# Optimization experiments

Measured on AMD Instinct MI355X. Metric: run time of the kernel, lower is better.

The kernel has to match this reference:

```python
import jax, jax.numpy as jnp
import numpy as np


def setup_inputs() -> dict:
    key = jax.random.key(0)
    B, S, D = 8, 2048, 1024
    inputs = jax.random.normal(key, (B, S, D), dtype=jnp.float32)
    return {"inputs": inputs}


def reference(inputs):
    # scores = X X^T / seq_len  (source divides by dk = inputs.shape[-2], the seq dim)
    seq_len = inputs.shape[-2]
    scores = jnp.einsum('bsd,btd->bst', inputs, inputs) / seq_len
    scores = jax.nn.softmax(scores, axis=-1)
    # context is computed in the original but not returned; keep the matmul for fidelity
    context = jnp.einsum('bst,btd->bsd', scores, inputs)
    del context
    return (inputs, scores)
```

## Files before the change

### kernel.cpp

```cpp
#include <hip/hip_runtime.h>

typedef unsigned short ushort_t;
using short8 = __attribute__((ext_vector_type(8))) short;
using half4  = __attribute__((ext_vector_type(4))) _Float16;
using half8  = __attribute__((ext_vector_type(8))) _Float16;
using f32x4  = __attribute__((ext_vector_type(4))) float;

#define AS1 __attribute__((address_space(1)))
#define AS3 __attribute__((address_space(3)))

#define B_   8
#define S_   2048
#define D_   1024
#define NIN  (8UL * 2048UL * 1024UL)
#define PARTS 32
#define SROWB 8192UL
#define BATCHB (2048UL * SROWB)


__device__ __forceinline__ ushort_t f2bf(float f) {
    unsigned u = __float_as_uint(f);
    u += 0x7FFFu + ((u >> 16) & 1u);
    return (ushort_t)(u >> 16);
}

__global__ __launch_bounds__(256) void cvt_packed(const float* __restrict__ in,
                                                  char* sc) {
    size_t g = ((size_t)blockIdx.x * 256 + threadIdx.x) * 8;
    const float4* p = (const float4*)(in + g);
    float4 a = p[0], c = p[1];
    short8 r;
    r[0] = (short)f2bf(a.x); r[1] = (short)f2bf(a.y);
    r[2] = (short)f2bf(a.z); r[3] = (short)f2bf(a.w);
    r[4] = (short)f2bf(c.x); r[5] = (short)f2bf(c.y);
    r[6] = (short)f2bf(c.z); r[7] = (short)f2bf(c.w);
    size_t xrow = g >> 10;
    size_t col  = g & 1023;
    char* dst = sc + xrow * SROWB + 2048 + col * 2;
    *(short8*)dst = r;
}

__global__ __launch_bounds__(256, 2) void gemm_sym3(char* sc,
                                                    const float4* xin,
                                                    float4* xout) {
    __shared__ __align__(16) ushort_t sA[2][128 * 64];
    __shared__ __align__(16) ushort_t sB[2][128 * 64];

    const int lin = blockIdx.x;
    const int wg  = (lin & 7) * 136 + (lin >> 3);
    const int b   = wg / 136;
    int rem = wg % 136, ti = 0;
    while (rem >= 16 - ti) { rem -= 16 - ti; ++ti; }
    const int tj = ti + rem;
    const int tr = ti * 128, tc = tj * 128;

    char* Sb = sc + (size_t)b * BATCHB;

    const int tid  = threadIdx.x;
    const int lane = tid & 63;
    const int wid  = tid >> 6;
    const int wr = (wid >> 1) * 64;
    const int wc = (wid & 1) * 64;

    const bool docopy = (lin < 1024);
    const size_t cbase = (size_t)lin * 256 + tid;

    f32x4 acc[4][4] = {};
    float4 creg;

    const int srow_s = tid >> 3;
    const int cd     = tid & 7;
    const int rsel = lane & 15;
    const int g4   = lane >> 4;
    const int sw   = lane & 7;

    auto stage = [&](int s, int slot) {
#pragma unroll
        for (int j = 0; j < 4; ++j) {
            const int row = j * 32 + srow_s;
            const int csw = (cd ^ (row & 7)) << 4;
            const size_t rbA = (size_t)(tr + row) * SROWB + 2048 + (size_t)s * 128;
            const size_t rbB = (size_t)(tc + row) * SROWB + 2048 + (size_t)s * 128;
            __builtin_amdgcn_global_load_lds((const AS1 void*)(Sb + rbA + csw),
                (AS3 void*)((char*)&sA[slot][0] + j * 4096 + tid * 16), 16, 0, 0);
            __builtin_amdgcn_global_load_lds((const AS1 void*)(Sb + rbB + csw),
                (AS3 void*)((char*)&sB[slot][0] + j * 4096 + tid * 16), 16, 0, 0);
        }
    };

    stage(0, 0);
    stage(1, 1);
    asm volatile("s_waitcnt vmcnt(8)" ::: "memory");
    __builtin_amdgcn_s_barrier();

#pragma unroll
    for (int s = 0; s < 16; ++s) {
        const int slot = s & 1;

        short8 af[2][4], bfr[2][4];
#pragma unroll
        for (int kk = 0; kk < 2; ++kk) {
            const int cb = kk * 4 + g4;
            const int csw = (cb ^ sw) << 4;
#pragma unroll
            for (int m = 0; m < 4; ++m) {
                const int row = wr + m * 16 + rsel;
                af[kk][m] = *(const short8*)((const char*)&sA[slot][0] + row * 128 + csw);
            }
#pragma unroll
            for (int n = 0; n < 4; ++n) {
                const int row = wc + n * 16 + rsel;
                bfr[kk][n] = *(const short8*)((const char*)&sB[slot][0] + row * 128 + csw);
            }
        }
        asm volatile("s_waitcnt lgkmcnt(0)" ::: "memory");
        __builtin_amdgcn_s_barrier();

        if (s + 2 < 16) stage(s + 2, slot);

        if (docopy) {
            if (s > 0) xout[cbase + (size_t)(s - 1) * 262144] = creg;
            creg = xin[cbase + (size_t)s * 262144];
        }

        if (docopy) {
            if (s == 0)       asm volatile("s_waitcnt vmcnt(9)"  ::: "memory");
            else if (s == 1)  asm volatile("s_waitcnt vmcnt(11)" ::: "memory");
            else if (s < 14)  asm volatile("s_waitcnt vmcnt(12)" ::: "memory");
            else if (s == 14) asm volatile("s_waitcnt vmcnt(4)"  ::: "memory");
        } else {
            if (s + 2 < 16)   asm volatile("s_waitcnt vmcnt(8)"  ::: "memory");
            else if (s == 14) asm volatile("s_waitcnt vmcnt(0)"  ::: "memory");
        }
        __builtin_amdgcn_s_barrier();

        __builtin_amdgcn_s_setprio(1);
#pragma unroll
        for (int kk = 0; kk < 2; ++kk)
#pragma unroll
            for (int m = 0; m < 4; ++m)
#pragma unroll
                for (int n = 0; n < 4; ++n)
                    acc[m][n] = __builtin_amdgcn_mfma_f32_16x16x32_bf16(
                        af[kk][m], bfr[kk][n], acc[m][n], 0, 0, 0);
        __builtin_amdgcn_s_setprio(0);
    }

    if (docopy) xout[cbase + 15UL * 262144] = creg;

    const float scale = 1.0f / 2048.0f;
    const int r0 = (lane >> 4) * 4;
    const int c0 = lane & 15;

#pragma unroll
    for (int m = 0; m < 4; ++m)
#pragma unroll
        for (int n = 0; n < 4; ++n)
#pragma unroll
            for (int rr = 0; rr < 4; ++rr)
                acc[m][n][rr] = __expf(acc[m][n][rr] * scale);

#pragma unroll
    for (int m = 0; m < 4; ++m) {
#pragma unroll
        for (int n = 0; n < 4; ++n) {
            char* dbase = Sb + (size_t)(tr + wr + m * 16 + r0) * SROWB + 4096
                             + (size_t)(tc + wc + n * 16 + c0) * 2;
#pragma unroll
            for (int rr = 0; rr < 4; ++rr)
                *(_Float16*)(dbase + (size_t)rr * SROWB) = (_Float16)acc[m][n][rr];
        }
    }

#pragma unroll
    for (int m = 0; m < 4; ++m) {
#pragma unroll
        for (int rr = 0; rr < 4; ++rr) {
            float s = (acc[m][0][rr] + acc[m][1][rr]) + (acc[m][2][rr] + acc[m][3][rr]);
            s += __shfl_xor(s, 1, 64);
            s += __shfl_xor(s, 2, 64);
            s += __shfl_xor(s, 4, 64);
            s += __shfl_xor(s, 8, 64);
            if ((lane & 15) == 0) {
                char* prow = Sb + (size_t)(tr + wr + m * 16 + r0 + rr) * SROWB;
                ((float*)prow)[tj * 2 + (wid & 1)] = s;
            }
        }
    }

    if (ti != tj) {
#pragma unroll
        for (int m = 0; m < 4; ++m) {
#pragma unroll
            for (int n = 0; n < 4; ++n) {
                half4 h;
#pragma unroll
                for (int rr = 0; rr < 4; ++rr) h[rr] = (_Float16)acc[m][n][rr];
                char* mb = Sb + (size_t)(tc + wc + n * 16 + c0) * SROWB + 4096
                              + (size_t)(tr + wr + m * 16 + r0) * 2;
                *(half4*)mb = h;
            }
        }
#pragma unroll
        for (int n = 0; n < 4; ++n) {
            float s = 0.0f;
#pragma unroll
            for (int m = 0; m < 4; ++m)
#pragma unroll
                for (int rr = 0; rr < 4; ++rr) s += acc[m][n][rr];
            s += __shfl_xor(s, 16, 64);
            s += __shfl_xor(s, 32, 64);
            if (lane < 16) {
                char* prow = Sb + (size_t)(tc + wc + n * 16 + lane) * SROWB;
                ((float*)prow)[ti * 2 + (wid >> 1)] = s;
            }
        }
    }
}

__global__ __launch_bounds__(256) void normalize_rows(char* sc) {
    const int row  = blockIdx.x * 4 + (threadIdx.x >> 6);
    const int lane = threadIdx.x & 63;
    char* rowc = sc + (size_t)row * SROWB;
    const _Float16* e = (const _Float16*)(rowc + 4096);
    float* s = (float*)rowc;

    float p = (lane < PARTS) ? ((const float*)rowc)[lane] : 0.0f;
#pragma unroll
    for (int o = 32; o > 0; o >>= 1) p += __shfl_xor(p, o, 64);
    const float inv = 1.0f / p;

    half8 v[4];
#pragma unroll
    for (int c = 0; c < 4; ++c)
        v[c] = *(const half8*)(e + c * 512 + lane * 8);

#pragma unroll
    for (int c = 0; c < 4; ++c) {
        float4 f0, f1;
        f0.x = (float)v[c][0] * inv; f0.y = (float)v[c][1] * inv;
        f0.z = (float)v[c][2] * inv; f0.w = (float)v[c][3] * inv;
        f1.x = (float)v[c][4] * inv; f1.y = (float)v[c][5] * inv;
        f1.z = (float)v[c][6] * inv; f1.w = (float)v[c][7] * inv;
        *(float4*)(s + c * 512 + lane * 8)     = f0;
        *(float4*)(s + c * 512 + lane * 8 + 4) = f1;
    }
}

extern "C" void kernel_launch(void* const* d_in, const int* in_sizes, int n_in,
                              void* d_out, int out_size, void* d_ws, size_t ws_size,
                              hipStream_t stream) {
    const float* X = (const float*)d_in[0];
    float* out = (float*)d_out;
    char*  sc  = (char*)d_out + NIN * 4;

    cvt_packed<<<NIN / (256 * 8), 256, 0, stream>>>(X, sc);
    gemm_sym3<<<1088, 256, 0, stream>>>(sc, (const float4*)X, (float4*)out);
    normalize_rows<<<(B_ * S_) / 4, 256, 0, stream>>>(sc);
}
```

Before: 118.8 us.

## Enlarge symmetric GEMM tiles to 256x256 with 512-thread workgroups

```diff
diff --git a/kernel.cpp b/kernel.cpp
--- a/kernel.cpp
+++ b/kernel.cpp
@@ -27,8 +27,8 @@
 __global__ __launch_bounds__(256) void cvt_packed(const float* __restrict__ in,
                                                   char* sc) {
     size_t g = ((size_t)blockIdx.x * 256 + threadIdx.x) * 8;
-    const float4* p = (const float4*)(in + g);
-    float4 a = p[0], c = p[1];
+    const f32x4* p = (const f32x4*)(in + g);
+    f32x4 a = p[0], c = p[1];
     short8 r;
     r[0] = (short)f2bf(a.x); r[1] = (short)f2bf(a.y);
     r[2] = (short)f2bf(a.z); r[3] = (short)f2bf(a.w);
@@ -40,52 +40,79 @@
     *(short8*)dst = r;
 }
 
-__global__ __launch_bounds__(256, 2) void gemm_sym3(char* sc,
-                                                    const float4* xin,
-                                                    float4* xout) {
-    __shared__ __align__(16) ushort_t sA[2][128 * 64];
-    __shared__ __align__(16) ushort_t sB[2][128 * 64];
+__global__ __launch_bounds__(512, 2) void gemm_sym7(char* sc,
+                                                    const f32x4* xin,
+                                                    f32x4* xout) {
+    __shared__ __align__(16) ushort_t sA[2][256 * 64];
+    __shared__ __align__(16) ushort_t sB[2][256 * 64];
 
     const int lin = blockIdx.x;
-    const int wg  = (lin & 7) * 136 + (lin >> 3);
-    const int b   = wg / 136;
-    int rem = wg % 136, ti = 0;
-    while (rem >= 16 - ti) { rem -= 16 - ti; ++ti; }
+    const int wg  = (lin & 7) * 36 + (lin >> 3);
+    const int b   = wg / 36;
+    int rem = wg % 36, ti = 0;
+    while (rem >= 8 - ti) { rem -= 8 - ti; ++ti; }
     const int tj = ti + rem;
-    const int tr = ti * 128, tc = tj * 128;
+    const int tr = ti * 256, tc = tj * 256;
 
     char* Sb = sc + (size_t)b * BATCHB;
 
     const int tid  = threadIdx.x;
     const int lane = tid & 63;
     const int wid  = tid >> 6;
-    const int wr = (wid >> 1) * 64;
-    const int wc = (wid & 1) * 64;
-
-    const bool docopy = (lin < 1024);
-    const size_t cbase = (size_t)lin * 256 + tid;
-
-    f32x4 acc[4][4] = {};
-    float4 creg;
+    const int wrow = (wid >> 2) * 128;
+    const int wcol = (wid & 3) * 64;
+
+    const bool docopy = (lin < 256);
+    const size_t cbase = (size_t)lin * 512 + tid;
+
+    f32x4 acc[8][4] = {};
+    f32x4 creg0, creg1;
 
     const int srow_s = tid >> 3;
     const int cd     = tid & 7;
     const int rsel = lane & 15;
     const int g4   = lane >> 4;
-    const int sw   = lane & 7;
 
     auto stage = [&](int s, int slot) {
 #pragma unroll
         for (int j = 0; j < 4; ++j) {
-            const int row = j * 32 + srow_s;
+            const int row = j * 64 + srow_s;
             const int csw = (cd ^ (row & 7)) << 4;
-            const size_t rbA = (size_t)(tr + row) * SROWB + 2048 + (size_t)s * 128;
-            const size_t rbB = (size_t)(tc + row) * SROWB + 2048 + (size_t)s * 128;
-            __builtin_amdgcn_global_load_lds((const AS1 void*)(Sb + rbA + csw),
-                (AS3 void*)((char*)&sA[slot][0] + j * 4096 + tid * 16), 16, 0, 0);
-            __builtin_amdgcn_global_load_lds((const AS1 void*)(Sb + rbB + csw),
-                (AS3 void*)((char*)&sB[slot][0] + j * 4096 + tid * 16), 16, 0, 0);
-        }
+            __builtin_amdgcn_global_load_lds(
+                (const AS1 void*)(Sb + (size_t)(tr + row) * SROWB + 2048 + (size_t)s * 128 + csw),
+                (AS3 void*)((char*)&sA[slot][0] + j * 8192 + tid * 16), 16, 0, 0);
+        }
+#pragma unroll
+        for (int j = 0; j < 4; ++j) {
+            const int row = j * 64 + srow_s;
+            const int csw = (cd ^ (row & 7)) << 4;
+            __builtin_amdgcn_global_load_lds(
+                (const AS1 void*)(Sb + (size_t)(tc + row) * SROWB + 2048 + (size_t)s * 128 + csw),
+                (AS3 void*)((char*)&sB[slot][0] + j * 8192 + tid * 16), 16, 0, 0);
+        }
+    };
+
+    short8 af[8], bfr[4];
+    auto readfrags = [&](int slot, int kk) {
+        const int cb  = kk * 4 + g4;
+#pragma unroll
+        for (int m = 0; m < 8; ++m) {
+            const int row = wrow + m * 16 + rsel;
+            af[m] = *(const short8*)((const char*)&sA[slot][0] + row * 128 + ((cb ^ (row & 7)) << 4));
+        }
+#pragma unroll
+        for (int n = 0; n < 4; ++n) {
+            const int row = wcol + n * 16 + rsel;
+            bfr[n] = *(const short8*)((const char*)&sB[slot][0] + row * 128 + ((cb ^ (row & 7)) << 4));
+        }
+    };
+    auto mfma32 = [&]() {
+#pragma unroll
+        for (int m = 0; m < 8; ++m)
+#pragma unroll
+            for (int n = 0; n < 4; ++n)
+                acc[m][n] = __builtin_amdgcn_mfma_f32_16x16x32_bf16(
+                    af[m], bfr[n], acc[m][n], 0, 0, 0);
     };
 
     stage(0, 0);
@@ -97,37 +124,34 @@
     for (int s = 0; s < 16; ++s) {
         const int slot = s & 1;
 
-        short8 af[2][4], bfr[2][4];
-#pragma unroll
-        for (int kk = 0; kk < 2; ++kk) {
-            const int cb = kk * 4 + g4;
-            const int csw = (cb ^ sw) << 4;
-#pragma unroll
-            for (int m = 0; m < 4; ++m) {
-                const int row = wr + m * 16 + rsel;
-                af[kk][m] = *(const short8*)((const char*)&sA[slot][0] + row * 128 + csw);
-            }
-#pragma unroll
-            for (int n = 0; n < 4; ++n) {
-                const int row = wc + n * 16 + rsel;
-                bfr[kk][n] = *(const short8*)((const char*)&sB[slot][0] + row * 128 + csw);
-            }
-        }
+        readfrags(slot, 0);
         asm volatile("s_waitcnt lgkmcnt(0)" ::: "memory");
+        __builtin_amdgcn_sched_barrier(0);
+        __builtin_amdgcn_s_setprio(1);
+        mfma32();
+        __builtin_amdgcn_s_setprio(0);
+
+        readfrags(slot, 1);
+        asm volatile("s_waitcnt lgkmcnt(0)" ::: "memory");
+        __builtin_amdgcn_sched_barrier(0);
         __builtin_amdgcn_s_barrier();
 
         if (s + 2 < 16) stage(s + 2, slot);
 
         if (docopy) {
-            if (s > 0) xout[cbase + (size_t)(s - 1) * 262144] = creg;
-            creg = xin[cbase + (size_t)s * 262144];
+            if (s > 0) {
+                xout[cbase + (size_t)(s - 1) * 262144]          = creg0;
+                xout[cbase + (size_t)(s - 1) * 262144 + 131072] = creg1;
+            }
+            creg0 = xin[cbase + (size_t)s * 262144];
+            creg1 = xin[cbase + (size_t)s * 262144 + 131072];
         }
 
         if (docopy) {
-            if (s == 0)       asm volatile("s_waitcnt vmcnt(9)"  ::: "memory");
-            else if (s == 1)  asm volatile("s_waitcnt vmcnt(11)" ::: "memory");
-            else if (s < 14)  asm volatile("s_waitcnt vmcnt(12)" ::: "memory");
-            else if (s == 14) asm volatile("s_waitcnt vmcnt(4)"  ::: "memory");
+            if (s == 0)       asm volatile("s_waitcnt vmcnt(10)" ::: "memory");
+            else if (s == 1)  asm volatile("s_waitcnt vmcnt(14)" ::: "memory");
+            else if (s < 14)  asm volatile("s_waitcnt vmcnt(16)" ::: "memory");
+            else if (s == 14) asm volatile("s_waitcnt vmcnt(8)"  ::: "memory");
         } else {
             if (s + 2 < 16)   asm volatile("s_waitcnt vmcnt(8)"  ::: "memory");
             else if (s == 14) asm volatile("s_waitcnt vmcnt(0)"  ::: "memory");
@@ -135,25 +159,21 @@
         __builtin_amdgcn_s_barrier();
 
         __builtin_amdgcn_s_setprio(1);
-#pragma unroll
-        for (int kk = 0; kk < 2; ++kk)
-#pragma unroll
-            for (int m = 0; m < 4; ++m)
-#pragma unroll
-                for (int n = 0; n < 4; ++n)
-                    acc[m][n] = __builtin_amdgcn_mfma_f32_16x16x32_bf16(
-                        af[kk][m], bfr[kk][n], acc[m][n], 0, 0, 0);
+        mfma32();
         __builtin_amdgcn_s_setprio(0);
     }
 
-    if (docopy) xout[cbase + 15UL * 262144] = creg;
+    if (docopy) {
+        xout[cbase + 15UL * 262144]          = creg0;
+        xout[cbase + 15UL * 262144 + 131072] = creg1;
+    }
 
     const float scale = 1.0f / 2048.0f;
     const int r0 = (lane >> 4) * 4;
     const int c0 = lane & 15;
 
 #pragma unroll
-    for (int m = 0; m < 4; ++m)
+    for (int m = 0; m < 8; ++m)
 #pragma unroll
         for (int n = 0; n < 4; ++n)
 #pragma unroll
@@ -161,11 +181,11 @@
                 acc[m][n][rr] = __expf(acc[m][n][rr] * scale);
 
 #pragma unroll
-    for (int m = 0; m < 4; ++m) {
+    for (int m = 0; m < 8; ++m) {
 #pragma unroll
         for (int n = 0; n < 4; ++n) {
-            char* dbase = Sb + (size_t)(tr + wr + m * 16 + r0) * SROWB + 4096
-                             + (size_t)(tc + wc + n * 16 + c0) * 2;
+            char* dbase = Sb + (size_t)(tr + wrow + m * 16 + r0) * SROWB + 4096
+                             + (size_t)(tc + wcol + n * 16 + c0) * 2;
 #pragma unroll
             for (int rr = 0; rr < 4; ++rr)
                 *(_Float16*)(dbase + (size_t)rr * SROWB) = (_Float16)acc[m][n][rr];
@@ -173,7 +193,7 @@
     }
 
 #pragma unroll
-    for (int m = 0; m < 4; ++m) {
+    for (int m = 0; m < 8; ++m) {
 #pragma unroll
         for (int rr = 0; rr < 4; ++rr) {
             float s = (acc[m][0][rr] + acc[m][1][rr]) + (acc[m][2][rr] + acc[m][3][rr]);
@@ -182,37 +202,42 @@
             s += __shfl_xor(s, 4, 64);
             s += __shfl_xor(s, 8, 64);
             if ((lane & 15) == 0) {
-                char* prow = Sb + (size_t)(tr + wr + m * 16 + r0 + rr) * SROWB;
-                ((float*)prow)[tj * 2 + (wid & 1)] = s;
+                char* prow = Sb + (size_t)(tr + wrow + m * 16 + r0 + rr) * SROWB;
+                ((float*)prow)[tj * 4 + (wid & 3)] = s;
             }
         }
     }
 
     if (ti != tj) {
 #pragma unroll
-        for (int m = 0; m < 4; ++m) {
+        for (int m = 0; m < 8; ++m) {
 #pragma unroll
             for (int n = 0; n < 4; ++n) {
                 half4 h;
 #pragma unroll
                 for (int rr = 0; rr < 4; ++rr) h[rr] = (_Float16)acc[m][n][rr];
-                char* mb = Sb + (size_t)(tc + wc + n * 16 + c0) * SROWB + 4096
-                              + (size_t)(tr + wr + m * 16 + r0) * 2;
+                char* mb = Sb + (size_t)(tc + wcol + n * 16 + c0) * SROWB + 4096
+                              + (size_t)(tr + wrow + m * 16 + r0) * 2;
                 *(half4*)mb = h;
             }
         }
 #pragma unroll
         for (int n = 0; n < 4; ++n) {
-            float s = 0.0f;
+            float s0 = 0.0f, s1 = 0.0f;
 #pragma unroll
             for (int m = 0; m < 4; ++m)
 #pragma unroll
-                for (int rr = 0; rr < 4; ++rr) s += acc[m][n][rr];
-            s += __shfl_xor(s, 16, 64);
-            s += __shfl_xor(s, 32, 64);
+                for (int rr = 0; rr < 4; ++rr) s0 += acc[m][n][rr];
+#pragma unroll
+            for (int m = 4; m < 8; ++m)
+#pragma unroll
+                for (int rr = 0; rr < 4; ++rr) s1 += acc[m][n][rr];
+            s0 += __shfl_xor(s0, 16, 64); s0 += __shfl_xor(s0, 32, 64);
+            s1 += __shfl_xor(s1, 16, 64); s1 += __shfl_xor(s1, 32, 64);
             if (lane < 16) {
-                char* prow = Sb + (size_t)(tc + wc + n * 16 + lane) * SROWB;
-                ((float*)prow)[ti * 2 + (wid >> 1)] = s;
+                char* prow = Sb + (size_t)(tc + wcol + n * 16 + lane) * SROWB;
+                ((float*)prow)[ti * 4 + (wid >> 2) * 2 + 0] = s0;
+                ((float*)prow)[ti * 4 + (wid >> 2) * 2 + 1] = s1;
             }
         }
     }
@@ -251,10 +276,9 @@
                               void* d_out, int out_size, void* d_ws, size_t ws_size,
                               hipStream_t stream) {
     const float* X = (const float*)d_in[0];
-    float* out = (float*)d_out;
     char*  sc  = (char*)d_out + NIN * 4;
 
     cvt_packed<<<NIN / (256 * 8), 256, 0, stream>>>(X, sc);
-    gemm_sym3<<<1088, 256, 0, stream>>>(sc, (const float4*)X, (float4*)out);
+    gemm_sym7<<<288, 512, 0, stream>>>(sc, (const f32x4*)X, (f32x4*)d_out);
     normalize_rows<<<(B_ * S_) / 4, 256, 0, stream>>>(sc);
 }
```

Measured after the change: 146.3 us. 1.23x slower.

## Deepen GEMM LDS pipeline to four stages with K=32 slices and single barrier

Applied to the files above, without the earlier changes.

```diff
diff --git a/kernel.cpp b/kernel.cpp
--- a/kernel.cpp
+++ b/kernel.cpp
@@ -27,8 +27,8 @@
 __global__ __launch_bounds__(256) void cvt_packed(const float* __restrict__ in,
                                                   char* sc) {
     size_t g = ((size_t)blockIdx.x * 256 + threadIdx.x) * 8;
-    const float4* p = (const float4*)(in + g);
-    float4 a = p[0], c = p[1];
+    const f32x4* p = (const f32x4*)(in + g);
+    f32x4 a = p[0], c = p[1];
     short8 r;
     r[0] = (short)f2bf(a.x); r[1] = (short)f2bf(a.y);
     r[2] = (short)f2bf(a.z); r[3] = (short)f2bf(a.w);
@@ -40,11 +40,11 @@
     *(short8*)dst = r;
 }
 
-__global__ __launch_bounds__(256, 2) void gemm_sym3(char* sc,
-                                                    const float4* xin,
-                                                    float4* xout) {
-    __shared__ __align__(16) ushort_t sA[2][128 * 64];
-    __shared__ __align__(16) ushort_t sB[2][128 * 64];
+__global__ __launch_bounds__(256, 2) void gemm_sym8(char* sc,
+                                                    const f32x4* xin,
+                                                    f32x4* xout) {
+    __shared__ __align__(16) ushort_t sA[4][128 * 32];
+    __shared__ __align__(16) ushort_t sB[4][128 * 32];
 
     const int lin = blockIdx.x;
     const int wg  = (lin & 7) * 136 + (lin >> 3);
@@ -62,91 +62,95 @@
     const int wr = (wid >> 1) * 64;
     const int wc = (wid & 1) * 64;
 
-    const bool docopy = (lin < 1024);
+    const bool docopy = (lin < 512);
     const size_t cbase = (size_t)lin * 256 + tid;
 
     f32x4 acc[4][4] = {};
-    float4 creg;
-
-    const int srow_s = tid >> 3;
-    const int cd     = tid & 7;
+    f32x4 creg;
+
+    const int srow_s = tid >> 2;
+    const int cd     = tid & 3;
     const int rsel = lane & 15;
     const int g4   = lane >> 4;
-    const int sw   = lane & 7;
 
     auto stage = [&](int s, int slot) {
 #pragma unroll
-        for (int j = 0; j < 4; ++j) {
-            const int row = j * 32 + srow_s;
-            const int csw = (cd ^ (row & 7)) << 4;
-            const size_t rbA = (size_t)(tr + row) * SROWB + 2048 + (size_t)s * 128;
-            const size_t rbB = (size_t)(tc + row) * SROWB + 2048 + (size_t)s * 128;
-            __builtin_amdgcn_global_load_lds((const AS1 void*)(Sb + rbA + csw),
+        for (int j = 0; j < 2; ++j) {
+            const int row = j * 64 + srow_s;
+            const int csw = (cd ^ ((row >> 1) & 3)) << 4;
+            __builtin_amdgcn_global_load_lds(
+                (const AS1 void*)(Sb + (size_t)(tr + row) * SROWB + 2048 + (size_t)s * 64 + csw),
                 (AS3 void*)((char*)&sA[slot][0] + j * 4096 + tid * 16), 16, 0, 0);
-            __builtin_amdgcn_global_load_lds((const AS1 void*)(Sb + rbB + csw),
+        }
+#pragma unroll
+        for (int j = 0; j < 2; ++j) {
+            const int row = j * 64 + srow_s;
+            const int csw = (cd ^ ((row >> 1) & 3)) << 4;
+            __builtin_amdgcn_global_load_lds(
+                (const AS1 void*)(Sb + (size_t)(tc + row) * SROWB + 2048 + (size_t)s * 64 + csw),
                 (AS3 void*)((char*)&sB[slot][0] + j * 4096 + tid * 16), 16, 0, 0);
+        }
+    };
+
+    short8 af[4], bfr[4];
+    auto readfrags = [&](int slot) {
+#pragma unroll
+        for (int m = 0; m < 4; ++m) {
+            const int row = wr + m * 16 + rsel;
+            const int csw = (g4 ^ ((row >> 1) & 3)) << 4;
+            af[m] = *(const short8*)((const char*)&sA[slot][0] + row * 64 + csw);
+        }
+#pragma unroll
+        for (int n = 0; n < 4; ++n) {
+            const int row = wc + n * 16 + rsel;
+            const int csw = (g4 ^ ((row >> 1) & 3)) << 4;
+            bfr[n] = *(const short8*)((const char*)&sB[slot][0] + row * 64 + csw);
         }
     };
 
     stage(0, 0);
     stage(1, 1);
-    asm volatile("s_waitcnt vmcnt(8)" ::: "memory");
-    __builtin_amdgcn_s_barrier();
-
-#pragma unroll
-    for (int s = 0; s < 16; ++s) {
-        const int slot = s & 1;
-
-        short8 af[2][4], bfr[2][4];
-#pragma unroll
-        for (int kk = 0; kk < 2; ++kk) {
-            const int cb = kk * 4 + g4;
-            const int csw = (cb ^ sw) << 4;
-#pragma unroll
-            for (int m = 0; m < 4; ++m) {
-                const int row = wr + m * 16 + rsel;
-                af[kk][m] = *(const short8*)((const char*)&sA[slot][0] + row * 128 + csw);
-            }
-#pragma unroll
-            for (int n = 0; n < 4; ++n) {
-                const int row = wc + n * 16 + rsel;
-                bfr[kk][n] = *(const short8*)((const char*)&sB[slot][0] + row * 128 + csw);
-            }
-        }
+    stage(2, 2);
+
+#pragma unroll
+    for (int s = 0; s < 32; ++s) {
+        if (docopy) {
+            if (s == 0)       asm volatile("s_waitcnt vmcnt(8)"  ::: "memory");
+            else if (s == 1)  asm volatile("s_waitcnt vmcnt(9)"  ::: "memory");
+            else if (s == 2)  asm volatile("s_waitcnt vmcnt(11)" ::: "memory");
+            else if (s == 3)  asm volatile("s_waitcnt vmcnt(13)" ::: "memory");
+            else if (s <= 29) asm volatile("s_waitcnt vmcnt(14)" ::: "memory");
+            else if (s == 30) asm volatile("s_waitcnt vmcnt(10)" ::: "memory");
+            else              asm volatile("s_waitcnt vmcnt(6)"  ::: "memory");
+        } else {
+            if (s <= 29)      asm volatile("s_waitcnt vmcnt(8)"  ::: "memory");
+            else if (s == 30) asm volatile("s_waitcnt vmcnt(4)"  ::: "memory");
+            else              asm volatile("s_waitcnt vmcnt(0)"  ::: "memory");
+        }
+        __builtin_amdgcn_s_barrier();
+
+        if (s + 3 < 32) stage(s + 3, (s + 3) & 3);
+
+        if (docopy) {
+            if (s > 0) xout[cbase + (size_t)(s - 1) * 131072] = creg;
+            creg = xin[cbase + (size_t)s * 131072];
+        }
+
+        readfrags(s & 3);
         asm volatile("s_waitcnt lgkmcnt(0)" ::: "memory");
-        __builtin_amdgcn_s_barrier();
-
-        if (s + 2 < 16) stage(s + 2, slot);
-
-        if (docopy) {
-            if (s > 0) xout[cbase + (size_t)(s - 1) * 262144] = creg;
-            creg = xin[cbase + (size_t)s * 262144];
-        }
-
-        if (docopy) {
-            if (s == 0)       asm volatile("s_waitcnt vmcnt(9)"  ::: "memory");
-            else if (s == 1)  asm volatile("s_waitcnt vmcnt(11)" ::: "memory");
-            else if (s < 14)  asm volatile("s_waitcnt vmcnt(12)" ::: "memory");
-            else if (s == 14) asm volatile("s_waitcnt vmcnt(4)"  ::: "memory");
-        } else {
-            if (s + 2 < 16)   asm volatile("s_waitcnt vmcnt(8)"  ::: "memory");
-            else if (s == 14) asm volatile("s_waitcnt vmcnt(0)"  ::: "memory");
-        }
-        __builtin_amdgcn_s_barrier();
+        __builtin_amdgcn_sched_barrier(0);
 
         __builtin_amdgcn_s_setprio(1);
 #pragma unroll
-        for (int kk = 0; kk < 2; ++kk)
-#pragma unroll
-            for (int m = 0; m < 4; ++m)
-#pragma unroll
-                for (int n = 0; n < 4; ++n)
-                    acc[m][n] = __builtin_amdgcn_mfma_f32_16x16x32_bf16(
-                        af[kk][m], bfr[kk][n], acc[m][n], 0, 0, 0);
+        for (int m = 0; m < 4; ++m)
+#pragma unroll
+            for (int n = 0; n < 4; ++n)
+                acc[m][n] = __builtin_amdgcn_mfma_f32_16x16x32_bf16(
+                    af[m], bfr[n], acc[m][n], 0, 0, 0);
         __builtin_amdgcn_s_setprio(0);
     }
 
-    if (docopy) xout[cbase + 15UL * 262144] = creg;
+    if (docopy) xout[cbase + 31UL * 131072] = creg;
 
     const float scale = 1.0f / 2048.0f;
     const int r0 = (lane >> 4) * 4;
@@ -251,10 +255,9 @@
                               void* d_out, int out_size, void* d_ws, size_t ws_size,
                               hipStream_t stream) {
     const float* X = (const float*)d_in[0];
-    float* out = (float*)d_out;
     char*  sc  = (char*)d_out + NIN * 4;
 
     cvt_packed<<<NIN / (256 * 8), 256, 0, stream>>>(X, sc);
-    gemm_sym3<<<1088, 256, 0, stream>>>(sc, (const float4*)X, (float4*)out);
+    gemm_sym8<<<1088, 256, 0, stream>>>(sc, (const f32x4*)X, (f32x4*)d_out);
     normalize_rows<<<(B_ * S_) / 4, 256, 0, stream>>>(sc);
 }
```

Result: slower. 135.3 us (+13.9%).

## Fuse row normalization into GEMM via per-row-block completion counters

Applied to the files above, without the earlier changes.

```diff
diff --git a/kernel.cpp b/kernel.cpp
--- a/kernel.cpp
+++ b/kernel.cpp
@@ -26,6 +26,10 @@
 
 __global__ __launch_bounds__(256) void cvt_packed(const float* __restrict__ in,
                                                   char* sc) {
+    if (blockIdx.x == 0 && threadIdx.x < 128) {
+        int b = threadIdx.x >> 4, g = threadIdx.x & 15;
+        *(int*)(sc + (size_t)b * BATCHB + (size_t)(g * 128) * SROWB + 128) = 0;
+    }
     size_t g = ((size_t)blockIdx.x * 256 + threadIdx.x) * 8;
     const float4* p = (const float4*)(in + g);
     float4 a = p[0], c = p[1];
@@ -40,11 +44,12 @@
     *(short8*)dst = r;
 }
 
-__global__ __launch_bounds__(256, 2) void gemm_sym3(char* sc,
+__global__ __launch_bounds__(256, 2) void gemm_sym9(char* sc,
                                                     const float4* xin,
                                                     float4* xout) {
     __shared__ __align__(16) ushort_t sA[2][128 * 64];
     __shared__ __align__(16) ushort_t sB[2][128 * 64];
+    __shared__ int sOwn[2];
 
     const int lin = blockIdx.x;
     const int wg  = (lin & 7) * 136 + (lin >> 3);
@@ -82,9 +87,9 @@
             const size_t rbA = (size_t)(tr + row) * SROWB + 2048 + (size_t)s * 128;
             const size_t rbB = (size_t)(tc + row) * SROWB + 2048 + (size_t)s * 128;
             __builtin_amdgcn_global_load_lds((const AS1 void*)(Sb + rbA + csw),
-                (AS3 void*)((char*)&sA[slot][0] + j * 4096 + tid * 16), 16, 0, 0);
+                (AS3 void*)((char*)&sA[slot][0] + j * 4096 + tid * 8 * 2), 16, 0, 0);
             __builtin_amdgcn_global_load_lds((const AS1 void*)(Sb + rbB + csw),
-                (AS3 void*)((char*)&sB[slot][0] + j * 4096 + tid * 16), 16, 0, 0);
+                (AS3 void*)((char*)&sB[slot][0] + j * 4096 + tid * 8 * 2), 16, 0, 0);
         }
     };
 
@@ -142,7 +147,8 @@
 #pragma unroll
                 for (int n = 0; n < 4; ++n)
                     acc[m][n] = __builtin_amdgcn_mfma_f32_16x16x32_bf16(
-                        af[kk][m], bfr[kk][n], acc[m][n], 0, 0, 0);
+                        af[kk][m], bfr[kk][n], acc[kk ? m : m][n], 0, 0, 0),
+                    acc[m][n] = acc[m][n];
         __builtin_amdgcn_s_setprio(0);
     }
 
@@ -216,34 +222,53 @@
             }
         }
     }
-}
-
-__global__ __launch_bounds__(256) void normalize_rows(char* sc) {
-    const int row  = blockIdx.x * 4 + (threadIdx.x >> 6);
-    const int lane = threadIdx.x & 63;
-    char* rowc = sc + (size_t)row * SROWB;
-    const _Float16* e = (const _Float16*)(rowc + 4096);
-    float* s = (float*)rowc;
-
-    float p = (lane < PARTS) ? ((const float*)rowc)[lane] : 0.0f;
-#pragma unroll
-    for (int o = 32; o > 0; o >>= 1) p += __shfl_xor(p, o, 64);
-    const float inv = 1.0f / p;
-
-    half8 v[4];
-#pragma unroll
-    for (int c = 0; c < 4; ++c)
-        v[c] = *(const half8*)(e + c * 512 + lane * 8);
-
-#pragma unroll
-    for (int c = 0; c < 4; ++c) {
-        float4 f0, f1;
-        f0.x = (float)v[c][0] * inv; f0.y = (float)v[c][1] * inv;
-        f0.z = (float)v[c][2] * inv; f0.w = (float)v[c][3] * inv;
-        f1.x = (float)v[c][4] * inv; f1.y = (float)v[c][5] * inv;
-        f1.z = (float)v[c][6] * inv; f1.w = (float)v[c][7] * inv;
-        *(float4*)(s + c * 512 + lane * 8)     = f0;
-        *(float4*)(s + c * 512 + lane * 8 + 4) = f1;
+
+    __syncthreads();
+    if (tid == 0) {
+        __threadfence();
+        int* c0p = (int*)(Sb + (size_t)(ti * 128) * SROWB + 128);
+        sOwn[0] = (atomicAdd(c0p, 1) == 15) ? 1 : 0;
+        if (ti != tj) {
+            int* c1p = (int*)(Sb + (size_t)(tj * 128) * SROWB + 128);
+            sOwn[1] = (atomicAdd(c1p, 1) == 15) ? 1 : 0;
+        } else {
+            sOwn[1] = 0;
+        }
+    }
+    __syncthreads();
+
+#pragma unroll
+    for (int which = 0; which < 2; ++which) {
+        if (!sOwn[which]) continue;
+        __threadfence();
+        const int g = which ? tj : ti;
+        for (int it = 0; it < 32; ++it) {
+            const int row = g * 128 + it * 4 + wid;
+            char* rowc = Sb + (size_t)row * SROWB;
+            const _Float16* e = (const _Float16*)(rowc + 4096);
+            float* so = (float*)rowc;
+
+            float p = (lane < PARTS) ? ((const float*)rowc)[lane] : 0.0f;
+#pragma unroll
+            for (int o = 32; o > 0; o >>= 1) p += __shfl_xor(p, o, 64);
+            const float inv = 1.0f / p;
+
+            half8 v[4];
+#pragma unroll
+            for (int c = 0; c < 4; ++c)
+                v[c] = *(const half8*)(e + c * 512 + lane * 8);
+
+#pragma unroll
+            for (int c = 0; c < 4; ++c) {
+                float4 f0, f1;
+                f0.x = (float)v[c][0] * inv; f0.y = (float)v[c][1] * inv;
+                f0.z = (float)v[c][2] * inv; f0.w = (float)v[c][3] * inv;
+                f1.x = (float)v[c][4] * inv; f1.y = (float)v[c][5] * inv;
+                f1.z = (float)v[c][6] * inv; f1.w = (float)v[c][7] * inv;
+                *(float4*)(so + c * 512 + lane * 8)     = f0;
+                *(float4*)(so + c * 512 + lane * 8 + 4) = f1;
+            }
+        }
     }
 }
 
@@ -251,10 +276,8 @@
                               void* d_out, int out_size, void* d_ws, size_t ws_size,
                               hipStream_t stream) {
     const float* X = (const float*)d_in[0];
-    float* out = (float*)d_out;
     char*  sc  = (char*)d_out + NIN * 4;
 
     cvt_packed<<<NIN / (256 * 8), 256, 0, stream>>>(X, sc);
-    gemm_sym3<<<1088, 256, 0, stream>>>(sc, (const float4*)X, (float4*)out);
-    normalize_rows<<<(B_ * S_) / 4, 256, 0, stream>>>(sc);
-}
+    gemm_sym9<<<1088, 256, 0, stream>>>(sc, (const float4*)X, (float4*)d_out);
+}
```

After: 245.5 us. +106.6%, slower.
